# Kernel optimization log

Hardware: AMD Instinct MI355X
Metric: run time of the kernel (lower is better)

## Reference

```python
import jax, jax.numpy as jnp
import numpy as np

N, C, H, W_ = 256, 64, 32, 32
IN_F = H * W_   # 1024
OUT_F = 1024

def setup_inputs() -> dict:
    key = jax.random.key(0)
    k1, k2, k3 = jax.random.split(key, 3)
    x = jax.random.normal(k1, (N, C, H, W_), dtype=jnp.float32)
    # per-channel Linear weights: (C, out_features, in_features), bias (C, out_features)
    scale = 1.0 / np.sqrt(IN_F)
    W = jax.random.uniform(k2, (C, OUT_F, IN_F), dtype=jnp.float32, minval=-scale, maxval=scale)
    b = jax.random.uniform(k3, (C, OUT_F), dtype=jnp.float32, minval=-scale, maxval=scale)
    return {"x": x, "W": W, "b": b}

def reference(x, W, b):
    n, c = x.shape[0], x.shape[1]
    z = x.reshape(n, c, -1)                      # (N, C, X)
    # sort each channel's vector in descending order (sort=True)
    z = -jnp.sort(-z, axis=-1)
    # grouped per-channel GEMM: y[n,c,o] = sum_x z[n,c,x] * W[c,o,x] + b[c,o]
    y = jnp.einsum('ncx,cox->nco', z, W) + b[None, :, :]
    return jax.nn.sigmoid(y)
```

## Files before the change

kernel.cpp:

```cpp
#include <hip/hip_runtime.h>

typedef _Float16 half8   __attribute__((ext_vector_type(8)));
typedef __fp16   half2_t __attribute__((ext_vector_type(2)));
typedef float    floatx4 __attribute__((ext_vector_type(4)));

__global__ __launch_bounds__(256) void sort_kernel(const float* __restrict__ x,
                                                   unsigned short* __restrict__ zs) {
  const int wave = threadIdx.x >> 6;
  const int lane = threadIdx.x & 63;
  const int vec  = (blockIdx.x << 2) + wave;

  const float* src = x + ((size_t)vec << 10) + (lane << 4);
  float v[16];
#pragma unroll
  for (int r4 = 0; r4 < 4; ++r4) {
    float4 f = *reinterpret_cast<const float4*>(src + (r4 << 2));
    v[r4 * 4 + 0] = f.x; v[r4 * 4 + 1] = f.y;
    v[r4 * 4 + 2] = f.z; v[r4 * 4 + 3] = f.w;
  }

  auto CEs = [&](int a, int b, bool desc) {
    float lo = fminf(v[a], v[b]);
    float hi = fmaxf(v[a], v[b]);
    v[a] = desc ? hi : lo;
    v[b] = desc ? lo : hi;
  };

#pragma unroll
  for (int r = 0; r < 16; r += 2) CEs(r, r + 1, (r & 2) == 0);
#pragma unroll
  for (int r = 0; r < 16; ++r) if ((r & 2) == 0) CEs(r, r | 2, (r & 4) == 0);
#pragma unroll
  for (int r = 0; r < 16; r += 2) CEs(r, r + 1, (r & 4) == 0);
#pragma unroll
  for (int r = 0; r < 16; ++r) if ((r & 4) == 0) CEs(r, r | 4, (r & 8) == 0);
#pragma unroll
  for (int r = 0; r < 16; ++r) if ((r & 2) == 0) CEs(r, r | 2, (r & 8) == 0);
#pragma unroll
  for (int r = 0; r < 16; r += 2) CEs(r, r + 1, (r & 8) == 0);

#pragma unroll
  for (int k = 16; k <= 1024; k <<= 1) {
    const bool d = (lane & (k >> 4)) == 0;
#pragma unroll
    for (int j = k >> 1; j >= 16; j >>= 1) {
      const int dl = j >> 4;
      const bool keepmax = (((lane & dl) == 0) == d);
#pragma unroll
      for (int r = 0; r < 16; ++r) {
        float p = __shfl_xor(v[r], dl, 64);
        v[r] = keepmax ? fmaxf(v[r], p) : fminf(v[r], p);
      }
    }
#pragma unroll
    for (int j = 8; j >= 1; j >>= 1)
#pragma unroll
      for (int r = 0; r < 16; ++r)
        if ((r & j) == 0) CEs(r, r | j, d);
  }

  const int n = vec >> 6, c = vec & 63;
  union { half2_t h2[8]; uint4 u[2]; } pk;
#pragma unroll
  for (int r = 0; r < 8; ++r)
    pk.h2[r] = __builtin_amdgcn_cvt_pkrtz(v[2 * r], v[2 * r + 1]);
  uint4* dst = reinterpret_cast<uint4*>(zs + ((size_t)(c * 256 + n) << 10) + (lane << 4));
  dst[0] = pk.u[0];
  dst[1] = pk.u[1];
}

__global__ __launch_bounds__(256) void gemm_kernel(const unsigned short* __restrict__ zs,
                                                   const float* __restrict__ W,
                                                   const float* __restrict__ bias,
                                                   float* __restrict__ out) {
  __shared__ unsigned short As[128 * 32];
  __shared__ unsigned short Bs[128 * 32];

  const int c    = blockIdx.y;
  const int t    = blockIdx.x;
  const int mt   = t >> 3;
  const int nt   = t & 7;
  const int tid  = threadIdx.x;
  const int wave = tid >> 6, lane = tid & 63;
  const int wm   = wave & 1, wn = wave >> 1;
  const int lr   = lane & 15;
  const int q    = lane >> 4;

  const unsigned short* Zbase = zs + (((size_t)(c * 256 + mt * 128)) << 10);
  const float*          Wbase = W + ((size_t)c << 20) + ((size_t)(nt * 128) << 10);

  floatx4 acc[4][4] = {};

  for (int kb = 0; kb < 1024; kb += 32) {
#pragma unroll
    for (int id = tid; id < 512; id += 256) {
      const int r = id >> 2, c8 = id & 3;
      const int ck = c8 ^ ((r >> 1) & 3);
      const uint4 val =
          *reinterpret_cast<const uint4*>(Zbase + ((size_t)r << 10) + kb + (c8 << 3));
      *reinterpret_cast<uint4*>(&As[(r << 5) + (ck << 3)]) = val;
    }
#pragma unroll
    for (int id = tid; id < 512; id += 256) {
      const int r = id >> 2, c8 = id & 3;
      const int ck = c8 ^ ((r >> 1) & 3);
      const float* wp = Wbase + ((size_t)r << 10) + kb + (c8 << 3);
      const float4 f0 = *reinterpret_cast<const float4*>(wp);
      const float4 f1 = *reinterpret_cast<const float4*>(wp + 4);
      union { half2_t h2[4]; uint4 u; } pk;
      pk.h2[0] = __builtin_amdgcn_cvt_pkrtz(f0.x, f0.y);
      pk.h2[1] = __builtin_amdgcn_cvt_pkrtz(f0.z, f0.w);
      pk.h2[2] = __builtin_amdgcn_cvt_pkrtz(f1.x, f1.y);
      pk.h2[3] = __builtin_amdgcn_cvt_pkrtz(f1.z, f1.w);
      *reinterpret_cast<uint4*>(&Bs[(r << 5) + (ck << 3)]) = pk.u;
    }
    __syncthreads();

    half8 af[4], bf[4];
#pragma unroll
    for (int mi = 0; mi < 4; ++mi) {
      const int r = wm * 64 + mi * 16 + lr;
      const int ck = q ^ ((r >> 1) & 3);
      af[mi] = *reinterpret_cast<const half8*>(&As[(r << 5) + (ck << 3)]);
    }
#pragma unroll
    for (int ni = 0; ni < 4; ++ni) {
      const int r = wn * 64 + ni * 16 + lr;
      const int ck = q ^ ((r >> 1) & 3);
      bf[ni] = *reinterpret_cast<const half8*>(&Bs[(r << 5) + (ck << 3)]);
    }
#pragma unroll
    for (int mi = 0; mi < 4; ++mi)
#pragma unroll
      for (int ni = 0; ni < 4; ++ni)
        acc[mi][ni] =
            __builtin_amdgcn_mfma_f32_16x16x32_f16(af[mi], bf[ni], acc[mi][ni], 0, 0, 0);
    __syncthreads();
  }

#pragma unroll
  for (int ni = 0; ni < 4; ++ni) {
    const int col = nt * 128 + wn * 64 + ni * 16 + lr;
    const float bv = bias[(c << 10) + col];
#pragma unroll
    for (int mi = 0; mi < 4; ++mi) {
      const int row0 = mt * 128 + wm * 64 + mi * 16 + q * 4;
#pragma unroll
      for (int rr = 0; rr < 4; ++rr) {
        const float y = acc[mi][ni][rr] + bv;
        const float s = 1.0f / (1.0f + __expf(-y));
        out[((((size_t)(row0 + rr) << 6) + c) << 10) + col] = s;
      }
    }
  }
}

extern "C" void kernel_launch(void* const* d_in, const int* in_sizes, int n_in,
                              void* d_out, int out_size, void* d_ws, size_t ws_size,
                              hipStream_t stream) {
  const float* x    = (const float*)d_in[0];
  const float* W    = (const float*)d_in[1];
  const float* bias = (const float*)d_in[2];
  float*       out  = (float*)d_out;
  unsigned short* zs = (unsigned short*)d_ws;

  sort_kernel<<<4096, 256, 0, stream>>>(x, zs);
  gemm_kernel<<<dim3(16, 64), 256, 0, stream>>>(zs, W, bias, out);
}
```

Measured before the change: 580.6 us.

## Load GEMM tiles with direct global-to-LDS copies and retile to full M

The GEMM kernel now stages A (fp16 sorted activations) and B (fp32 weights) straight into LDS with global_load_lds 16-byte copies and XOR swizzling, instead of going through registers. Each block covers all 256 rows of a channel and 64 output columns, with K steps of 64. Weights stay fp32 in LDS and are converted to fp16 after the LDS read, just before the MFMA. This cuts register staging and means each weight tile is read from global memory only once, at the cost of more LDS traffic for fp32 B and a larger LDS footprint. The sigmoid now uses a hardware reciprocal.

```diff
diff --git a/kernel.cpp b/kernel.cpp
--- a/kernel.cpp
+++ b/kernel.cpp
@@ -3,6 +3,12 @@
 typedef _Float16 half8   __attribute__((ext_vector_type(8)));
 typedef __fp16   half2_t __attribute__((ext_vector_type(2)));
 typedef float    floatx4 __attribute__((ext_vector_type(4)));
+
+__device__ inline void async_copy16(const void* g, void* l) {
+  __builtin_amdgcn_global_load_lds(
+      (const __attribute__((address_space(1))) unsigned int*)g,
+      (__attribute__((address_space(3))) unsigned int*)l, 16, 0, 0);
+}
 
 __global__ __launch_bounds__(256) void sort_kernel(const float* __restrict__ x,
                                                    unsigned short* __restrict__ zs) {
@@ -73,83 +79,85 @@
                                                    const float* __restrict__ W,
                                                    const float* __restrict__ bias,
                                                    float* __restrict__ out) {
-  __shared__ unsigned short As[128 * 32];
-  __shared__ unsigned short Bs[128 * 32];
+  __shared__ unsigned short As[256 * 64];
+  __shared__ float          Bs[64 * 64];
 
   const int c    = blockIdx.y;
-  const int t    = blockIdx.x;
-  const int mt   = t >> 3;
-  const int nt   = t & 7;
+  const int nt   = blockIdx.x;
   const int tid  = threadIdx.x;
-  const int wave = tid >> 6, lane = tid & 63;
-  const int wm   = wave & 1, wn = wave >> 1;
+  const int w    = tid >> 6, lane = tid & 63;
   const int lr   = lane & 15;
   const int q    = lane >> 4;
 
-  const unsigned short* Zbase = zs + (((size_t)(c * 256 + mt * 128)) << 10);
-  const float*          Wbase = W + ((size_t)c << 20) + ((size_t)(nt * 128) << 10);
+  const unsigned short* zc = zs + (((size_t)c * 256) << 10);
+  const float*          wc = W + ((size_t)c << 20) + (((size_t)nt * 64) << 10);
+
+  const int a_lr8 = lane >> 3, a_ch = lane & 7;
+  const int a_cs  = a_ch ^ a_lr8;
+  const int b_lr4 = lane >> 4, b_ch = lane & 15;
+  const int b_cs  = b_ch ^ ((4 * (w & 1) + b_lr4) & 7);
 
   floatx4 acc[4][4] = {};
+  union U { uint4 u; half8 h; float4 f; };
 
-  for (int kb = 0; kb < 1024; kb += 32) {
+  for (int kb = 0; kb < 1024; kb += 64) {
 #pragma unroll
-    for (int id = tid; id < 512; id += 256) {
-      const int r = id >> 2, c8 = id & 3;
-      const int ck = c8 ^ ((r >> 1) & 3);
-      const uint4 val =
-          *reinterpret_cast<const uint4*>(Zbase + ((size_t)r << 10) + kb + (c8 << 3));
-      *reinterpret_cast<uint4*>(&As[(r << 5) + (ck << 3)]) = val;
+    for (int p = 0; p < 8; ++p) {
+      const int r0 = (p * 4 + w) * 8;
+      const unsigned short* g =
+          zc + (((size_t)(r0 + a_lr8)) << 10) + kb + (a_cs << 3);
+      async_copy16(g, &As[r0 << 6]);
     }
 #pragma unroll
-    for (int id = tid; id < 512; id += 256) {
-      const int r = id >> 2, c8 = id & 3;
-      const int ck = c8 ^ ((r >> 1) & 3);
-      const float* wp = Wbase + ((size_t)r << 10) + kb + (c8 << 3);
-      const float4 f0 = *reinterpret_cast<const float4*>(wp);
-      const float4 f1 = *reinterpret_cast<const float4*>(wp + 4);
-      union { half2_t h2[4]; uint4 u; } pk;
-      pk.h2[0] = __builtin_amdgcn_cvt_pkrtz(f0.x, f0.y);
-      pk.h2[1] = __builtin_amdgcn_cvt_pkrtz(f0.z, f0.w);
-      pk.h2[2] = __builtin_amdgcn_cvt_pkrtz(f1.x, f1.y);
-      pk.h2[3] = __builtin_amdgcn_cvt_pkrtz(f1.z, f1.w);
-      *reinterpret_cast<uint4*>(&Bs[(r << 5) + (ck << 3)]) = pk.u;
+    for (int p = 0; p < 4; ++p) {
+      const int o0 = (p * 4 + w) * 4;
+      const float* g = wc + (((size_t)(o0 + b_lr4)) << 10) + kb + (b_cs << 2);
+      async_copy16(g, &Bs[o0 << 6]);
     }
     __syncthreads();
 
-    half8 af[4], bf[4];
 #pragma unroll
-    for (int mi = 0; mi < 4; ++mi) {
-      const int r = wm * 64 + mi * 16 + lr;
-      const int ck = q ^ ((r >> 1) & 3);
-      af[mi] = *reinterpret_cast<const half8*>(&As[(r << 5) + (ck << 3)]);
+    for (int ks = 0; ks < 2; ++ks) {
+      half8 af[4];
+#pragma unroll
+      for (int mi = 0; mi < 4; ++mi) {
+        const int r  = w * 64 + mi * 16 + lr;
+        const int ch = (ks * 4 + q) ^ (r & 7);
+        af[mi] = *reinterpret_cast<const half8*>(&As[(r << 6) + (ch << 3)]);
+      }
+#pragma unroll
+      for (int ni = 0; ni < 4; ++ni) {
+        const int o  = ni * 16 + lr;
+        const int c0 = (ks * 8 + q * 2) ^ (o & 7);
+        const int c1 = (ks * 8 + q * 2 + 1) ^ (o & 7);
+        const float4 f0 = *reinterpret_cast<const float4*>(&Bs[(o << 6) + (c0 << 2)]);
+        const float4 f1 = *reinterpret_cast<const float4*>(&Bs[(o << 6) + (c1 << 2)]);
+        union { half2_t h2[4]; half8 h8; } pk;
+        pk.h2[0] = __builtin_amdgcn_cvt_pkrtz(f0.x, f0.y);
+        pk.h2[1] = __builtin_amdgcn_cvt_pkrtz(f0.z, f0.w);
+        pk.h2[2] = __builtin_amdgcn_cvt_pkrtz(f1.x, f1.y);
+        pk.h2[3] = __builtin_amdgcn_cvt_pkrtz(f1.z, f1.w);
+#pragma unroll
+        for (int mi = 0; mi < 4; ++mi)
+          acc[mi][ni] =
+              __builtin_amdgcn_mfma_f32_16x16x32_f16(af[mi], pk.h8, acc[mi][ni], 0, 0, 0);
+      }
     }
-#pragma unroll
-    for (int ni = 0; ni < 4; ++ni) {
-      const int r = wn * 64 + ni * 16 + lr;
-      const int ck = q ^ ((r >> 1) & 3);
-      bf[ni] = *reinterpret_cast<const half8*>(&Bs[(r << 5) + (ck << 3)]);
-    }
-#pragma unroll
-    for (int mi = 0; mi < 4; ++mi)
-#pragma unroll
-      for (int ni = 0; ni < 4; ++ni)
-        acc[mi][ni] =
-            __builtin_amdgcn_mfma_f32_16x16x32_f16(af[mi], bf[ni], acc[mi][ni], 0, 0, 0);
     __syncthreads();
   }
 
 #pragma unroll
   for (int ni = 0; ni < 4; ++ni) {
-    const int col = nt * 128 + wn * 64 + ni * 16 + lr;
+    const int col = nt * 64 + ni * 16 + lr;
     const float bv = bias[(c << 10) + col];
 #pragma unroll
     for (int mi = 0; mi < 4; ++mi) {
-      const int row0 = mt * 128 + wm * 64 + mi * 16 + q * 4;
+      const int row0 = w * 64 + mi * 16 + q * 4;
 #pragma unroll
       for (int rr = 0; rr < 4; ++rr) {
         const float y = acc[mi][ni][rr] + bv;
-        const float s = 1.0f / (1.0f + __expf(-y));
-        out[((((size_t)(row0 + rr) << 6) + c) << 10) + col] = s;
+        const float s = __builtin_amdgcn_rcpf(1.0f + __expf(-y));
+        out[(((size_t)(row0 + rr) << 6) + c) * 1024 + col] = s;
       }
     }
   }
```

Result: faster. 482.1 us (-17.0%).
